# Optimization experiments

Hardware: AMD Instinct MI355X
Metric: run time of the kernel (lower is better)

Reference implementation:

```python
import jax, jax.numpy as jnp
import numpy as np

B = 8          # events per batch
NPB = 8192     # points per event (equal counts -> Nmax = NPB)
N = B * NPB
FEAT = 6
K = 128        # max_tokens
TOK = 768      # token_dim
KNN = 16       # k_neighbors
MLP_DIMS = [FEAT, 256, 512, 768, TOK]


def setup_inputs() -> dict:
    key = jax.random.key(0)
    ks = jax.random.split(key, 20)
    coords = jax.random.normal(ks[0], (N, 3), jnp.float32) * 5.0
    features = jax.random.normal(ks[1], (N, FEAT), jnp.float32)
    times = jax.random.uniform(ks[2], (N, 1), jnp.float32)
    # equal-sized, sorted batch ids (8192 points per event)
    batch_ids = jnp.repeat(jnp.arange(B, dtype=jnp.int32), NPB)
    inp = {"coords": coords, "features": features, "batch_ids": batch_ids, "times": times}
    # per-point MLP: 6 -> 256 -> 512 -> 768 -> 768 (last Linear has no ReLU)
    ki = 3
    for i in range(4):
        din, dout = MLP_DIMS[i], MLP_DIMS[i + 1]
        inp[f"W{i+1}"] = jax.random.normal(ks[ki], (din, dout), jnp.float32) / np.sqrt(din); ki += 1
        inp[f"b{i+1}"] = jnp.zeros((dout,), jnp.float32)
    # neighborhood MLP: 768 -> 768 -> 768
    inp["Wn1"] = jax.random.normal(ks[ki], (TOK, TOK), jnp.float32) / np.sqrt(TOK); ki += 1
    inp["bn1"] = jnp.zeros((TOK,), jnp.float32)
    inp["Wn2"] = jax.random.normal(ks[ki], (TOK, TOK), jnp.float32) / np.sqrt(TOK); ki += 1
    inp["bn2"] = jnp.zeros((TOK,), jnp.float32)
    return inp


def _forward(coords, features, batch_ids, times,
             W1, b1, W2, b2, W3, b3, W4, b4, Wn1, bn1, Wn2, bn2):
    INF = jnp.float32(jnp.inf)
    points4 = jnp.concatenate([coords[:, :3], times], axis=-1)  # [N,4] (x,y,z,t)
    # per-point MLP
    h = jax.nn.relu(features @ W1 + b1)
    h = jax.nn.relu(h @ W2 + b2)
    h = jax.nn.relu(h @ W3 + b3)
    feats = h @ W4 + b4                                          # [N,TOK]
    # ---- pack flat -> padded [B, NPB, *] ----
    counts = jnp.bincount(batch_ids, length=B)                   # [B]
    offsets = jnp.cumsum(counts) - counts
    pos = jnp.arange(N) - offsets[batch_ids]
    P = jnp.zeros((B, NPB, 4), points4.dtype).at[batch_ids, pos].set(points4)
    Fp = jnp.zeros((B, NPB, TOK), feats.dtype).at[batch_ids, pos].set(feats)
    valid = jnp.arange(NPB)[None, :] < counts[:, None]           # [B,NPB]
    # ---- small path: take first K points sorted by time ----
    tsort = jnp.where(valid, P[..., 3], INF)
    sorted_idx = jnp.argsort(tsort, axis=1)[:, :K]               # K <= NPB
    tokens_small = jnp.take_along_axis(Fp, sorted_idx[..., None], axis=1)
    cents_small = jnp.take_along_axis(P, sorted_idx[..., None], axis=1)
    masks_small = jnp.arange(K)[None, :] < jnp.minimum(counts, K)[:, None]
    tokens_small = tokens_small * masks_small[..., None]
    cents_small = cents_small * masks_small[..., None]
    # ---- batched FPS over 4D points ----
    min_d0 = jnp.where(valid, INF, 0.0)
    norms = jnp.where(valid, jnp.sum(P * P, axis=-1), -INF)
    first = jnp.argmax(norms, axis=1)                            # farthest-from-origin start
    barange = jnp.arange(B)
    def fps_step(carry, _):
        min_d, last = carry
        c = P[barange, last]                                     # [B,4]
        d = jnp.sum((P - c[:, None, :]) ** 2, axis=-1)
        d = jnp.where(valid, d, INF)
        min_d = jnp.minimum(min_d, d)
        return (min_d, jnp.argmax(min_d, axis=1)), last
    _, idx_seq = jax.lax.scan(fps_step, (min_d0, first), None, length=K)
    fps_idx = idx_seq.T                                          # [B,K]
    validK = jnp.arange(K)[None, :] < jnp.minimum(counts, K)[:, None]
    cents_large = jnp.take_along_axis(P, fps_idx[..., None], axis=1)  # [B,K,4]
    # ---- kNN pooling around centroids ----
    diff = cents_large[:, :, None, :] - P[:, None, :, :]         # [B,K,NPB,4]
    dists = jnp.sum(diff * diff, axis=-1)                        # [B,K,NPB]
    dists = jnp.where(valid[:, None, :], dists, INF)
    k_g = min(KNN, NPB)
    _, knn_idx = jax.lax.top_k(-dists, k_g)                      # smallest-k -> [B,K,k]
    knn_valid = jnp.take_along_axis(jnp.broadcast_to(valid[:, None, :], (B, K, NPB)), knn_idx, axis=2)
    neigh = jnp.take_along_axis(Fp[:, None, :, :], knn_idx[..., None], axis=2)  # [B,K,k,TOK]
    masked = jnp.where(knn_valid[..., None], neigh, -INF)
    pooled = jnp.max(masked, axis=2)
    pooled = jnp.where(jnp.isfinite(pooled), pooled, 0.0)
    tokens_large = jax.nn.relu(pooled @ Wn1 + bn1) @ Wn2 + bn2   # [B,K,TOK]
    # sort selected tokens by centroid time
    ctimes = jnp.where(validK, cents_large[..., 3], INF)
    order = jnp.argsort(ctimes, axis=1)
    tokens_large = jnp.take_along_axis(tokens_large, order[..., None], axis=1)
    cents_large = jnp.take_along_axis(cents_large, order[..., None], axis=1)
    masks_large = jnp.take_along_axis(validK, order, axis=1)
    tokens_large = tokens_large * masks_large[..., None]
    cents_large = cents_large * masks_large[..., None]
    # ---- select per-event path ----
    small = counts <= K
    tokens = jnp.where(small[:, None, None], tokens_small, tokens_large)
    cents = jnp.where(small[:, None, None], cents_small, cents_large)
    masks = jnp.where(small[:, None], masks_small, masks_large)
    return tokens, cents, masks


def reference(coords, features, batch_ids, times,
              W1, b1, W2, b2, W3, b3, W4, b4, Wn1, bn1, Wn2, bn2):
    return _forward(coords, features, batch_ids, times,
                    W1, b1, W2, b2, W3, b3, W4, b4, Wn1, bn1, Wn2, bn2)
```

## Files before the change

### kernel.cpp

```cpp
#include <hip/hip_runtime.h>
#include <hip/hip_bf16.h>


#define BEV 8
#define NPB 8192
#define FEAT 6
#define KTOK 128
#define TOK 768
#define KNN 16

typedef unsigned short ushort_t;
typedef unsigned long long u64;
typedef __bf16 bf16x8 __attribute__((ext_vector_type(8)));
typedef float f32x4 __attribute__((ext_vector_type(4)));
typedef float f32x2 __attribute__((ext_vector_type(2)));

__device__ __forceinline__ ushort_t f2b(float f) {
    union { float f; unsigned int i; } x; x.f = f;
    unsigned int i = x.i;
    unsigned int r = (i + 0x7FFFu + ((i >> 16) & 1u)) >> 16;
    return (ushort_t)r;
}

#define DPP_ROW_SHR1  0x111
#define DPP_ROW_SHR2  0x112
#define DPP_ROW_SHR4  0x114
#define DPP_ROW_SHR8  0x118
#define DPP_ROW_BC15  0x142
#define DPP_ROW_BC31  0x143

template <int CTRL>
__device__ __forceinline__ float dpp_fmax(float v) {
    int o = __builtin_amdgcn_update_dpp(__float_as_int(v), __float_as_int(v),
                                        CTRL, 0xf, 0xf, false);
    return fmaxf(v, __int_as_float(o));
}

template <int CTRL>
__device__ __forceinline__ u64 dpp_u64max(u64 k) {
    int lo = (int)(unsigned)(k & 0xFFFFFFFFu);
    int hi = (int)(unsigned)(k >> 32);
    unsigned olo = (unsigned)__builtin_amdgcn_update_dpp(lo, lo, CTRL, 0xf, 0xf, false);
    unsigned ohi = (unsigned)__builtin_amdgcn_update_dpp(hi, hi, CTRL, 0xf, 0xf, false);
    u64 o = ((u64)ohi << 32) | (u64)olo;
    return o > k ? o : k;
}

__global__ __launch_bounds__(256) void fill_kernel(float* __restrict__ out, int n) {
    int i = blockIdx.x * 256 + threadIdx.x;
    if (i < n) out[i] = 0.f;
}

__global__ __launch_bounds__(1024) void fps_kernel(
    const float* __restrict__ coords, const float* __restrict__ times,
    float* __restrict__ cents, int* __restrict__ pos,
    float* __restrict__ cents_out, float* __restrict__ masks_out)
{
#pragma clang fp contract(off)
    const int b = blockIdx.x;
    const int t = threadIdx.x;
    __shared__ u64   slotk[2][16];
    __shared__ __align__(16) float slotc[2][16][4];
    __shared__ float tarr[KTOK];
    __shared__ float carr[KTOK][4];
    f32x2 px[4], py[4], pz[4], pw[4], md[4];
    const long base = (long)b * NPB;
#pragma unroll
    for (int i = 0; i < 4; ++i) {
        long g = base + t * 8 + i * 2;
        px[i] = (f32x2){coords[g * 3 + 0], coords[(g + 1) * 3 + 0]};
        py[i] = (f32x2){coords[g * 3 + 1], coords[(g + 1) * 3 + 1]};
        pz[i] = (f32x2){coords[g * 3 + 2], coords[(g + 1) * 3 + 2]};
        pw[i] = (f32x2){times[g], times[g + 1]};
        md[i] = (f32x2){__builtin_inff(), __builtin_inff()};
    }
    const int wv = t >> 6, lane = t & 63;
    float cx = 0.f, cy = 0.f, cz = 0.f, cw = 0.f;
    for (int s = 0; s < KTOK; ++s) {
        float bv = -__builtin_inff(); int bi = t * 8;
        if (s == 0) {
#pragma unroll
            for (int i = 0; i < 4; ++i) {
                f32x2 n = ((px[i]*px[i] + py[i]*py[i]) + pz[i]*pz[i]) + pw[i]*pw[i];
                if (n[0] > bv) { bv = n[0]; bi = t * 8 + i * 2; }
                if (n[1] > bv) { bv = n[1]; bi = t * 8 + i * 2 + 1; }
            }
        } else {
            const f32x2 c2x = {cx, cx}, c2y = {cy, cy}, c2z = {cz, cz}, c2w = {cw, cw};
#pragma unroll
            for (int i = 0; i < 4; ++i) {
                f32x2 dx = px[i] - c2x, dy = py[i] - c2y;
                f32x2 dz = pz[i] - c2z, dw = pw[i] - c2w;
                f32x2 d = ((dx*dx + dy*dy) + dz*dz) + dw*dw;
                md[i] = __builtin_elementwise_min(md[i], d);
                if (md[i][0] > bv) { bv = md[i][0]; bi = t * 8 + i * 2; }
                if (md[i][1] > bv) { bv = md[i][1]; bi = t * 8 + i * 2 + 1; }
            }
        }
        float mvv = bv;
        mvv = dpp_fmax<DPP_ROW_SHR1>(mvv);
        mvv = dpp_fmax<DPP_ROW_SHR2>(mvv);
        mvv = dpp_fmax<DPP_ROW_SHR4>(mvv);
        mvv = dpp_fmax<DPP_ROW_SHR8>(mvv);
        mvv = dpp_fmax<DPP_ROW_BC15>(mvv);
        mvv = dpp_fmax<DPP_ROW_BC31>(mvv);
        const float mv = __int_as_float(__builtin_amdgcn_readlane(__float_as_int(mvv), 63));
        const u64 mask = __ballot(bv == mv);
        const int wl = __ffsll((long long)mask) - 1;
        const int p = s & 1;
        if (lane == wl) {
            slotk[p][wv] = ((u64)__float_as_uint(mv) << 32)
                         | (unsigned)(NPB - 1 - bi);
            const int ii = bi & 7;
            float sx = px[0][0], sy = py[0][0], sz = pz[0][0], sw = pw[0][0];
#pragma unroll
            for (int j = 1; j < 8; ++j)
                if (ii == j) { sx = px[j>>1][j&1]; sy = py[j>>1][j&1];
                               sz = pz[j>>1][j&1]; sw = pw[j>>1][j&1]; }
            slotc[p][wv][0] = sx; slotc[p][wv][1] = sy;
            slotc[p][wv][2] = sz; slotc[p][wv][3] = sw;
        }
        __syncthreads();
        u64 k1 = slotk[p][lane & 15];
        f32x4 c4 = *(const f32x4*)&slotc[p][lane & 15][0];
        k1 = dpp_u64max<DPP_ROW_SHR1>(k1);
        k1 = dpp_u64max<DPP_ROW_SHR2>(k1);
        k1 = dpp_u64max<DPP_ROW_SHR4>(k1);
        k1 = dpp_u64max<DPP_ROW_SHR8>(k1);
        const unsigned klo =
            (unsigned)__builtin_amdgcn_readlane((int)(unsigned)(k1 & 0xFFFFFFFFu), 15);
        const int widx = NPB - 1 - (int)klo;
        const int gw = widx >> 9;
        cx = __int_as_float(__builtin_amdgcn_readlane(__float_as_int(c4[0]), gw));
        cy = __int_as_float(__builtin_amdgcn_readlane(__float_as_int(c4[1]), gw));
        cz = __int_as_float(__builtin_amdgcn_readlane(__float_as_int(c4[2]), gw));
        cw = __int_as_float(__builtin_amdgcn_readlane(__float_as_int(c4[3]), gw));
        if (t == 0) {
            tarr[s] = cw;
            carr[s][0] = cx; carr[s][1] = cy; carr[s][2] = cz; carr[s][3] = cw;
        }
    }
    __syncthreads();
    if (t < KTOK) {
        const float ti = tarr[t];
        int rank = 0;
        for (int j = 0; j < KTOK; ++j) {
            float tj = tarr[j];
            if (tj < ti || (tj == ti && j < t)) ++rank;
        }
        rank &= (KTOK - 1);
        pos[b * KTOK + t] = rank;
        float* cc = &cents[(b * KTOK + t) * 4];
        cc[0] = carr[t][0]; cc[1] = carr[t][1];
        cc[2] = carr[t][2]; cc[3] = carr[t][3];
#pragma unroll
        for (int c = 0; c < 4; ++c)
            cents_out[(b * KTOK + rank) * 4 + c] = carr[t][c];
        masks_out[b * KTOK + t] = 1.0f;
    }
}

__global__ __launch_bounds__(256) void knn_kernel(
    const float* __restrict__ coords, const float* __restrict__ times,
    const float* __restrict__ cents, int* __restrict__ knn_idx)
{
#pragma clang fp contract(off)
    const int blk = blockIdx.x;
    const int b = blk >> 7;
    const int t = threadIdx.x;
    const float cx = cents[blk*4+0], cy = cents[blk*4+1];
    const float cz = cents[blk*4+2], cw = cents[blk*4+3];
    float d[32];
    const long base = (long)b * NPB;
#pragma unroll
    for (int i = 0; i < 32; ++i) {
        long g = base + t * 32 + i;
        float dx = coords[g*3+0] - cx;
        float dy = coords[g*3+1] - cy;
        float dz = coords[g*3+2] - cz;
        float dw = times[g] - cw;
        d[i] = ((dx*dx + dy*dy) + dz*dz) + dw*dw;
    }
    __shared__ float rv[4];
    __shared__ int   ri[4];
    const int wv = t >> 6, lane = t & 63;
    for (int pass = 0; pass < KNN; ++pass) {
        float bvv = __builtin_inff(); int bii = t * 32;
#pragma unroll
        for (int i = 0; i < 32; ++i)
            if (d[i] < bvv) { bvv = d[i]; bii = t * 32 + i; }
        for (int off = 1; off < 64; off <<= 1) {
            float ov = __shfl_xor(bvv, off);
            int   oi = __shfl_xor(bii, off);
            if (ov < bvv || (ov == bvv && oi < bii)) { bvv = ov; bii = oi; }
        }
        if (lane == 0) { rv[wv] = bvv; ri[wv] = bii; }
        __syncthreads();
        float gb = __builtin_inff(); int winner = 0;
        for (int wI = 0; wI < 4; ++wI) {
            float v = rv[wI]; int idx = ri[wI];
            if (v < gb || (v == gb && idx < winner)) { gb = v; winner = idx; }
        }
        winner &= (NPB - 1);
#pragma unroll
        for (int i = 0; i < 32; ++i)
            if (t * 32 + i == winner) d[i] = __builtin_inff();
        if (t == 0) knn_idx[blk * KNN + pass] = winner;
        __syncthreads();
    }
}

__global__ __launch_bounds__(256) void tc_all(
    const float* __restrict__ W2, ushort_t* __restrict__ Wt2,
    const float* __restrict__ W3, ushort_t* __restrict__ Wt3,
    const float* __restrict__ W4, ushort_t* __restrict__ Wt4)
{
    const float* in; ushort_t* out; int K, N;
    if (blockIdx.z == 0)      { in = W2; out = Wt2; K = 256; N = 512; }
    else if (blockIdx.z == 1) { in = W3; out = Wt3; K = 512; N = 768; }
    else                      { in = W4; out = Wt4; K = 768; N = 768; }
    if ((int)blockIdx.x * 32 >= N || (int)blockIdx.y * 32 >= K) return;
    __shared__ float tile[32][33];
    const int tx = threadIdx.x, ty = threadIdx.y;
#pragma unroll
    for (int r = 0; r < 4; ++r) {
        int y = blockIdx.y * 32 + ty + r * 8;
        tile[ty + r * 8][tx] = in[(long)y * N + blockIdx.x * 32 + tx];
    }
    __syncthreads();
    const int ko = blockIdx.y * 32 + tx;
#pragma unroll
    for (int r = 0; r < 4; ++r) {
        int no = blockIdx.x * 32 + ty + r * 8;
        out[(long)no * K + ko] = f2b(tile[tx][ty + r * 8]);
    }
}

#define PAD1 264
#define PAD2 520
#define PAD3 776
__global__ __launch_bounds__(256, 2) void mlp_fused(
    const float* __restrict__ features, const float* __restrict__ W1,
    const float* __restrict__ b1, const int* __restrict__ knn_idx,
    const ushort_t* __restrict__ Wt2, const float* __restrict__ b2,
    const ushort_t* __restrict__ Wt3, const float* __restrict__ b3,
    const ushort_t* __restrict__ Wt4, const float* __restrict__ b4,
    ushort_t* __restrict__ pooled)
{
    __shared__ __align__(16) ushort_t lds[35904];
    ushort_t* h1 = lds;
    ushort_t* h2 = lds + 8448;
    ushort_t* h3 = lds;
    ushort_t* Bs = lds + 25088;
    float*    feat = (float*)(lds + 35328);
    int*      pidx = (int*)(lds + 35840);

    const int bi = blockIdx.x;
    const int t = threadIdx.x;
    const int w = t >> 6, lane = t & 63;
    const int ln = lane & 15, q = lane >> 4;

    if (t < 32) {
        const int c = bi * 2 + (t >> 4);
        const int ev = c >> 7;
        pidx[t] = ev * NPB + (knn_idx[c * KNN + (t & 15)] & (NPB - 1));
    }
    __syncthreads();
    if (t < 192) {
        const int r = t / 6, f = t - r * 6;
        feat[r * 8 + f] = features[(long)pidx[r] * FEAT + f];
    }
    __syncthreads();
    {
        float wv[FEAT];
#pragma unroll
        for (int f = 0; f < FEAT; ++f) wv[f] = W1[f * 256 + t];
        const float bias = b1[t];
#pragma unroll
        for (int r = 0; r < 32; ++r) {
            float acc = 0.f;
#pragma unroll
            for (int f = 0; f < FEAT; ++f) acc += feat[r * 8 + f] * wv[f];
            h1[r * PAD1 + t] = f2b(fmaxf(acc + bias, 0.f));
        }
    }
    __syncthreads();

    {
        f32x4 acc[2][8];
#pragma unroll
        for (int m = 0; m < 2; ++m)
#pragma unroll
            for (int i = 0; i < 8; ++i) acc[m][i] = (f32x4){0,0,0,0};
        for (int k0 = 0; k0 < 256; k0 += 32) {
            bf16x8 af[2];
#pragma unroll
            for (int m = 0; m < 2; ++m)
                af[m] = *(const bf16x8*)(&h1[(m * 16 + ln) * PAD1 + k0 + q * 8]);
#pragma unroll
            for (int np = 0; np < 2; ++np) {
                __syncthreads();
#pragma unroll
                for (int i = 0; i < 4; ++i) {
                    int e = t + i * 256, n = e >> 2, sk = e & 3;
                    *(uint4*)(&Bs[n * 40 + sk * 8]) =
                        *(const uint4*)(Wt2 + (long)(np * 256 + n) * 256 + k0 + sk * 8);
                }
                __syncthreads();
#pragma unroll
                for (int j = 0; j < 4; ++j) {
                    bf16x8 bf = *(const bf16x8*)(&Bs[((w * 4 + j) * 16 + ln) * 40 + q * 8]);
#pragma unroll
                    for (int m = 0; m < 2; ++m)
                        acc[m][np * 4 + j] = __builtin_amdgcn_mfma_f32_16x16x32_bf16(af[m], bf, acc[m][np * 4 + j], 0, 0, 0);
                }
            }
        }
        __syncthreads();
#pragma unroll
        for (int np = 0; np < 2; ++np)
#pragma unroll
            for (int j = 0; j < 4; ++j) {
                const int col = np * 256 + (w * 4 + j) * 16 + ln;
                const float bias = b2[col];
#pragma unroll
                for (int m = 0; m < 2; ++m)
#pragma unroll
                    for (int r = 0; r < 4; ++r)
                        h2[(m * 16 + q * 4 + r) * PAD2 + col] = f2b(fmaxf(acc[m][np * 4 + j][r] + bias, 0.f));
            }
    }
    __syncthreads();

    {
        f32x4 acc[2][12];
#pragma unroll
        for (int m = 0; m < 2; ++m)
#pragma unroll
            for (int i = 0; i < 12; ++i) acc[m][i] = (f32x4){0,0,0,0};
        for (int k0 = 0; k0 < 512; k0 += 32) {
            bf16x8 af[2];
#pragma unroll
            for (int m = 0; m < 2; ++m)
                af[m] = *(const bf16x8*)(&h2[(m * 16 + ln) * PAD2 + k0 + q * 8]);
#pragma unroll
            for (int np = 0; np < 3; ++np) {
                __syncthreads();
#pragma unroll
                for (int i = 0; i < 4; ++i) {
                    int e = t + i * 256, n = e >> 2, sk = e & 3;
                    *(uint4*)(&Bs[n * 40 + sk * 8]) =
                        *(const uint4*)(Wt3 + (long)(np * 256 + n) * 512 + k0 + sk * 8);
                }
                __syncthreads();
#pragma unroll
                for (int j = 0; j < 4; ++j) {
                    bf16x8 bf = *(const bf16x8*)(&Bs[((w * 4 + j) * 16 + ln) * 40 + q * 8]);
#pragma unroll
                    for (int m = 0; m < 2; ++m)
                        acc[m][np * 4 + j] = __builtin_amdgcn_mfma_f32_16x16x32_bf16(af[m], bf, acc[m][np * 4 + j], 0, 0, 0);
                }
            }
        }
        __syncthreads();
#pragma unroll
        for (int np = 0; np < 3; ++np)
#pragma unroll
            for (int j = 0; j < 4; ++j) {
                const int col = np * 256 + (w * 4 + j) * 16 + ln;
                const float bias = b3[col];
#pragma unroll
                for (int m = 0; m < 2; ++m)
#pragma unroll
                    for (int r = 0; r < 4; ++r)
                        h3[(m * 16 + q * 4 + r) * PAD3 + col] = f2b(fmaxf(acc[m][np * 4 + j][r] + bias, 0.f));
            }
    }
    __syncthreads();

    {
        f32x4 acc[2][12];
#pragma unroll
        for (int m = 0; m < 2; ++m)
#pragma unroll
            for (int i = 0; i < 12; ++i) acc[m][i] = (f32x4){0,0,0,0};
        for (int k0 = 0; k0 < 768; k0 += 32) {
            bf16x8 af[2];
#pragma unroll
            for (int m = 0; m < 2; ++m)
                af[m] = *(const bf16x8*)(&h3[(m * 16 + ln) * PAD3 + k0 + q * 8]);
#pragma unroll
            for (int np = 0; np < 3; ++np) {
                __syncthreads();
#pragma unroll
                for (int i = 0; i < 4; ++i) {
                    int e = t + i * 256, n = e >> 2, sk = e & 3;
                    *(uint4*)(&Bs[n * 40 + sk * 8]) =
                        *(const uint4*)(Wt4 + (long)(np * 256 + n) * 768 + k0 + sk * 8);
                }
                __syncthreads();
#pragma unroll
                for (int j = 0; j < 4; ++j) {
                    bf16x8 bf = *(const bf16x8*)(&Bs[((w * 4 + j) * 16 + ln) * 40 + q * 8]);
#pragma unroll
                    for (int m = 0; m < 2; ++m)
                        acc[m][np * 4 + j] = __builtin_amdgcn_mfma_f32_16x16x32_bf16(af[m], bf, acc[m][np * 4 + j], 0, 0, 0);
                }
            }
        }
#pragma unroll
        for (int np = 0; np < 3; ++np)
#pragma unroll
            for (int j = 0; j < 4; ++j) {
                const int col = np * 256 + (w * 4 + j) * 16 + ln;
#pragma unroll
                for (int m = 0; m < 2; ++m) {
                    float v = fmaxf(fmaxf(acc[m][np * 4 + j][0], acc[m][np * 4 + j][1]),
                                    fmaxf(acc[m][np * 4 + j][2], acc[m][np * 4 + j][3]));
                    v = fmaxf(v, __shfl_xor(v, 16));
                    v = fmaxf(v, __shfl_xor(v, 32));
                    if (q == 0)
                        pooled[(long)(bi * 2 + m) * TOK + col] = f2b(v + b4[col]);
                }
            }
    }
}

template<int EPI, int RELU, int F32OUT>
__global__ __launch_bounds__(256) void gemm64_kn(
    const ushort_t* __restrict__ A, const float* __restrict__ B,
    const float* __restrict__ bias, void* __restrict__ Cv,
    int M, int N, int Kd, const int* __restrict__ pos)
{
    __shared__ __align__(16) ushort_t As[64 * 40];
    __shared__ __align__(16) ushort_t Bsh[64 * 40];
    ushort_t* Cb = (ushort_t*)Cv;
    float*    Cf = (float*)Cv;
    const int tid = threadIdx.x;
    const int m0 = blockIdx.x * 64;
    const int n0 = blockIdx.y * 64;
    const int w = tid >> 6, lane = tid & 63;
    const int ln = lane & 15, q = lane >> 4;
    f32x4 acc[4];
#pragma unroll
    for (int ni = 0; ni < 4; ++ni) acc[ni] = (f32x4){0.f, 0.f, 0.f, 0.f};

    const int ar = tid >> 2, as0 = (tid & 3) * 8;
    const int kk = tid >> 4, nn = (tid & 15) * 4;

    for (int k0 = 0; k0 < Kd; k0 += 32) {
        __syncthreads();
        uint4 a0 = *(const uint4*)(A + (long)(m0 + ar) * Kd + k0 + as0);
        float4 f0 = *(const float4*)(B + (long)(k0 + kk)      * N + n0 + nn);
        float4 f1 = *(const float4*)(B + (long)(k0 + kk + 16) * N + n0 + nn);
        *(uint4*)(&As[ar * 40 + as0]) = a0;
        float e0[4] = {f0.x, f0.y, f0.z, f0.w};
        float e1[4] = {f1.x, f1.y, f1.z, f1.w};
#pragma unroll
        for (int j = 0; j < 4; ++j) Bsh[(nn + j) * 40 + kk]      = f2b(e0[j]);
#pragma unroll
        for (int j = 0; j < 4; ++j) Bsh[(nn + j) * 40 + kk + 16] = f2b(e1[j]);
        __syncthreads();
        bf16x8 af = *(const bf16x8*)(&As[(w * 16 + ln) * 40 + q * 8]);
#pragma unroll
        for (int ni = 0; ni < 4; ++ni) {
            bf16x8 bf = *(const bf16x8*)(&Bsh[(ni * 16 + ln) * 40 + q * 8]);
            acc[ni] = __builtin_amdgcn_mfma_f32_16x16x32_bf16(af, bf, acc[ni], 0, 0, 0);
        }
    }

#pragma unroll
    for (int ni = 0; ni < 4; ++ni) {
        const int col = n0 + ni * 16 + ln;
        const float bv = bias[col];
#pragma unroll
        for (int r = 0; r < 4; ++r) {
            const int row = m0 + w * 16 + q * 4 + r;
            float v = acc[ni][r] + bv;
            if (EPI == 0) {
                if (RELU) v = fmaxf(v, 0.f);
                if (F32OUT) Cf[(long)row * N + col] = v;
                else        Cb[(long)row * N + col] = f2b(v);
            } else {
                const int orow = (row & ~(KTOK - 1)) + (pos[row] & (KTOK - 1));
                if (F32OUT) Cf[(long)orow * N + col] = v;
                else        Cb[(long)orow * N + col] = f2b(v);
            }
        }
    }
}

extern "C" void kernel_launch(void* const* d_in, const int* in_sizes, int n_in,
                              void* d_out, int out_size, void* d_ws, size_t ws_size,
                              hipStream_t stream)
{
    const float* coords   = (const float*)d_in[0];
    const float* features = (const float*)d_in[1];
    const float* times    = (const float*)d_in[3];
    const float* W1  = (const float*)d_in[4];
    const float* b1  = (const float*)d_in[5];
    const float* W2  = (const float*)d_in[6];
    const float* b2  = (const float*)d_in[7];
    const float* W3  = (const float*)d_in[8];
    const float* b3  = (const float*)d_in[9];
    const float* W4  = (const float*)d_in[10];
    const float* b4  = (const float*)d_in[11];
    const float* Wn1 = (const float*)d_in[12];
    const float* bn1 = (const float*)d_in[13];
    const float* Wn2 = (const float*)d_in[14];
    const float* bn2 = (const float*)d_in[15];

    char* ws = (char*)d_ws;
    float*    cents   = (float*)(ws + 0);
    int*      pos     = (int*)(ws + 16384);
    int*      knn_idx = (int*)(ws + 20480);
    ushort_t* t1      = (ushort_t*)(ws + 86016);
    ushort_t* pooled  = (ushort_t*)(ws + 1658880);
    ushort_t* Wt2b    = (ushort_t*)(ws + 3231744);
    ushort_t* Wt3b    = (ushort_t*)(ws + 3493888);
    ushort_t* Wt4b    = (ushort_t*)(ws + 4280320);
    const long WS_NEED = 5459968;

    float* tokens_out = (float*)d_out;
    float* cents_out  = tokens_out + 786432;
    float* masks_out  = tokens_out + 790528;

    if ((long)ws_size < WS_NEED) {
        fill_kernel<<<(791552 + 255) / 256, 256, 0, stream>>>(tokens_out, 791552);
        return;
    }

    tc_all<<<dim3(24, 24, 3), dim3(32, 8), 0, stream>>>(W2, Wt2b, W3, Wt3b, W4, Wt4b);

    fps_kernel<<<BEV, 1024, 0, stream>>>(coords, times, cents, pos, cents_out, masks_out);
    knn_kernel<<<BEV * KTOK, 256, 0, stream>>>(coords, times, cents, knn_idx);

    mlp_fused<<<512, 256, 0, stream>>>(features, W1, b1, knn_idx,
                                       Wt2b, b2, Wt3b, b3, Wt4b, b4, pooled);

    gemm64_kn<0,1,0><<<dim3(16, 12), 256, 0, stream>>>(pooled, Wn1, bn1, t1, 1024, 768, 768, nullptr);
    gemm64_kn<2,0,1><<<dim3(16, 12), 256, 0, stream>>>(t1, Wn2, bn2, tokens_out, 1024, 768, 768, pos);
}
```

Baseline: 478.3 us.

## Split FPS across four blocks per event with global atomic key exchange

```diff
diff --git a/kernel.cpp b/kernel.cpp
--- a/kernel.cpp
+++ b/kernel.cpp
@@ -8,6 +8,8 @@
 #define KTOK 128
 #define TOK 768
 #define KNN 16
+#define FPS_S 4
+#define FPS_KSTRIDE 16
 
 typedef unsigned short ushort_t;
 typedef unsigned long long u64;
@@ -53,49 +55,43 @@
 
 __global__ __launch_bounds__(1024) void fps_kernel(
     const float* __restrict__ coords, const float* __restrict__ times,
-    float* __restrict__ cents, int* __restrict__ pos,
+    float* __restrict__ cents, int* __restrict__ pos, u64* __restrict__ keys,
     float* __restrict__ cents_out, float* __restrict__ masks_out)
 {
 #pragma clang fp contract(off)
-    const int b = blockIdx.x;
+    const int blk = blockIdx.x;
+    const int b = blk >> 2, bl = blk & (FPS_S - 1);
     const int t = threadIdx.x;
     __shared__ u64   slotk[2][16];
-    __shared__ __align__(16) float slotc[2][16][4];
     __shared__ float tarr[KTOK];
     __shared__ float carr[KTOK][4];
-    f32x2 px[4], py[4], pz[4], pw[4], md[4];
     const long base = (long)b * NPB;
-#pragma unroll
-    for (int i = 0; i < 4; ++i) {
-        long g = base + t * 8 + i * 2;
-        px[i] = (f32x2){coords[g * 3 + 0], coords[(g + 1) * 3 + 0]};
-        py[i] = (f32x2){coords[g * 3 + 1], coords[(g + 1) * 3 + 1]};
-        pz[i] = (f32x2){coords[g * 3 + 2], coords[(g + 1) * 3 + 2]};
-        pw[i] = (f32x2){times[g], times[g + 1]};
-        md[i] = (f32x2){__builtin_inff(), __builtin_inff()};
-    }
+    const int g0 = bl * (NPB / FPS_S) + t * 2;
+    f32x2 px, py, pz, pw, md;
+    {
+        long g = base + g0;
+        px = (f32x2){coords[g * 3 + 0], coords[(g + 1) * 3 + 0]};
+        py = (f32x2){coords[g * 3 + 1], coords[(g + 1) * 3 + 1]};
+        pz = (f32x2){coords[g * 3 + 2], coords[(g + 1) * 3 + 2]};
+        pw = (f32x2){times[g], times[g + 1]};
+    }
+    md = (f32x2){__builtin_inff(), __builtin_inff()};
     const int wv = t >> 6, lane = t & 63;
     float cx = 0.f, cy = 0.f, cz = 0.f, cw = 0.f;
     for (int s = 0; s < KTOK; ++s) {
-        float bv = -__builtin_inff(); int bi = t * 8;
+        float bv; int bi = g0;
         if (s == 0) {
-#pragma unroll
-            for (int i = 0; i < 4; ++i) {
-                f32x2 n = ((px[i]*px[i] + py[i]*py[i]) + pz[i]*pz[i]) + pw[i]*pw[i];
-                if (n[0] > bv) { bv = n[0]; bi = t * 8 + i * 2; }
-                if (n[1] > bv) { bv = n[1]; bi = t * 8 + i * 2 + 1; }
-            }
+            f32x2 n = ((px*px + py*py) + pz*pz) + pw*pw;
+            bv = n[0];
+            if (n[1] > bv) { bv = n[1]; bi = g0 + 1; }
         } else {
             const f32x2 c2x = {cx, cx}, c2y = {cy, cy}, c2z = {cz, cz}, c2w = {cw, cw};
-#pragma unroll
-            for (int i = 0; i < 4; ++i) {
-                f32x2 dx = px[i] - c2x, dy = py[i] - c2y;
-                f32x2 dz = pz[i] - c2z, dw = pw[i] - c2w;
-                f32x2 d = ((dx*dx + dy*dy) + dz*dz) + dw*dw;
-                md[i] = __builtin_elementwise_min(md[i], d);
-                if (md[i][0] > bv) { bv = md[i][0]; bi = t * 8 + i * 2; }
-                if (md[i][1] > bv) { bv = md[i][1]; bi = t * 8 + i * 2 + 1; }
-            }
+            f32x2 dx = px - c2x, dy = py - c2y;
+            f32x2 dz = pz - c2z, dw = pw - c2w;
+            f32x2 d = ((dx*dx + dy*dy) + dz*dz) + dw*dw;
+            md = __builtin_elementwise_min(md, d);
+            bv = md[0];
+            if (md[1] > bv) { bv = md[1]; bi = g0 + 1; }
         }
         float mvv = bv;
         mvv = dpp_fmax<DPP_ROW_SHR1>(mvv);
@@ -108,40 +104,45 @@
         const u64 mask = __ballot(bv == mv);
         const int wl = __ffsll((long long)mask) - 1;
         const int p = s & 1;
-        if (lane == wl) {
-            slotk[p][wv] = ((u64)__float_as_uint(mv) << 32)
+        if (lane == wl)
+            slotk[p][wv] = ((u64)(__float_as_uint(mv) + 1u) << 32)
                          | (unsigned)(NPB - 1 - bi);
-            const int ii = bi & 7;
-            float sx = px[0][0], sy = py[0][0], sz = pz[0][0], sw = pw[0][0];
-#pragma unroll
-            for (int j = 1; j < 8; ++j)
-                if (ii == j) { sx = px[j>>1][j&1]; sy = py[j>>1][j&1];
-                               sz = pz[j>>1][j&1]; sw = pw[j>>1][j&1]; }
-            slotc[p][wv][0] = sx; slotc[p][wv][1] = sy;
-            slotc[p][wv][2] = sz; slotc[p][wv][3] = sw;
-        }
         __syncthreads();
         u64 k1 = slotk[p][lane & 15];
-        f32x4 c4 = *(const f32x4*)&slotc[p][lane & 15][0];
         k1 = dpp_u64max<DPP_ROW_SHR1>(k1);
         k1 = dpp_u64max<DPP_ROW_SHR2>(k1);
         k1 = dpp_u64max<DPP_ROW_SHR4>(k1);
         k1 = dpp_u64max<DPP_ROW_SHR8>(k1);
         const unsigned klo =
             (unsigned)__builtin_amdgcn_readlane((int)(unsigned)(k1 & 0xFFFFFFFFu), 15);
-        const int widx = NPB - 1 - (int)klo;
-        const int gw = widx >> 9;
-        cx = __int_as_float(__builtin_amdgcn_readlane(__float_as_int(c4[0]), gw));
-        cy = __int_as_float(__builtin_amdgcn_readlane(__float_as_int(c4[1]), gw));
-        cz = __int_as_float(__builtin_amdgcn_readlane(__float_as_int(c4[2]), gw));
-        cw = __int_as_float(__builtin_amdgcn_readlane(__float_as_int(c4[3]), gw));
+        const unsigned khi =
+            (unsigned)__builtin_amdgcn_readlane((int)(unsigned)(k1 >> 32), 15);
+        u64* kq = keys + (long)(s * BEV + b) * FPS_KSTRIDE;
+        if (t == 0)
+            __hip_atomic_store(&kq[bl], ((u64)khi << 32) | (u64)klo,
+                               __ATOMIC_RELAXED, __HIP_MEMORY_SCOPE_AGENT);
+        u64 q0, q1, q2, q3;
+        for (;;) {
+            q0 = __hip_atomic_load(&kq[0], __ATOMIC_RELAXED, __HIP_MEMORY_SCOPE_AGENT);
+            q1 = __hip_atomic_load(&kq[1], __ATOMIC_RELAXED, __HIP_MEMORY_SCOPE_AGENT);
+            q2 = __hip_atomic_load(&kq[2], __ATOMIC_RELAXED, __HIP_MEMORY_SCOPE_AGENT);
+            q3 = __hip_atomic_load(&kq[3], __ATOMIC_RELAXED, __HIP_MEMORY_SCOPE_AGENT);
+            if (q0 && q1 && q2 && q3) break;
+        }
+        u64 ka = q0 > q1 ? q0 : q1;
+        u64 kb2 = q2 > q3 ? q2 : q3;
+        u64 kg = ka > kb2 ? ka : kb2;
+        const int widx = NPB - 1 - (int)(unsigned)(kg & 0xFFFFFFFFu);
+        const long gc = base + widx;
+        cx = coords[gc * 3 + 0]; cy = coords[gc * 3 + 1];
+        cz = coords[gc * 3 + 2]; cw = times[gc];
         if (t == 0) {
             tarr[s] = cw;
             carr[s][0] = cx; carr[s][1] = cy; carr[s][2] = cz; carr[s][3] = cw;
         }
     }
     __syncthreads();
-    if (t < KTOK) {
+    if (bl == 0 && t < KTOK) {
         const float ti = tarr[t];
         int rank = 0;
         for (int j = 0; j < KTOK; ++j) {
@@ -213,8 +214,15 @@
 __global__ __launch_bounds__(256) void tc_all(
     const float* __restrict__ W2, ushort_t* __restrict__ Wt2,
     const float* __restrict__ W3, ushort_t* __restrict__ Wt3,
-    const float* __restrict__ W4, ushort_t* __restrict__ Wt4)
+    const float* __restrict__ W4, ushort_t* __restrict__ Wt4,
+    u64* __restrict__ keys)
 {
+    if (blockIdx.z == 3) {
+        int id = ((int)blockIdx.y * 24 + (int)blockIdx.x) * 256
+               + (int)threadIdx.y * 32 + (int)threadIdx.x;
+        if (id < KTOK * BEV * FPS_KSTRIDE) keys[id] = 0ull;
+        return;
+    }
     const float* in; ushort_t* out; int K, N;
     if (blockIdx.z == 0)      { in = W2; out = Wt2; K = 256; N = 512; }
     else if (blockIdx.z == 1) { in = W3; out = Wt3; K = 512; N = 768; }
@@ -519,7 +527,8 @@
     ushort_t* Wt2b    = (ushort_t*)(ws + 3231744);
     ushort_t* Wt3b    = (ushort_t*)(ws + 3493888);
     ushort_t* Wt4b    = (ushort_t*)(ws + 4280320);
-    const long WS_NEED = 5459968;
+    u64*      fpskeys = (u64*)(ws + 5459968);
+    const long WS_NEED = 5459968 + 131072;
 
     float* tokens_out = (float*)d_out;
     float* cents_out  = tokens_out + 786432;
@@ -530,9 +539,10 @@
         return;
     }
 
-    tc_all<<<dim3(24, 24, 3), dim3(32, 8), 0, stream>>>(W2, Wt2b, W3, Wt3b, W4, Wt4b);
-
-    fps_kernel<<<BEV, 1024, 0, stream>>>(coords, times, cents, pos, cents_out, masks_out);
+    tc_all<<<dim3(24, 24, 4), dim3(32, 8), 0, stream>>>(W2, Wt2b, W3, Wt3b, W4, Wt4b, fpskeys);
+
+    fps_kernel<<<BEV * FPS_S, 1024, 0, stream>>>(coords, times, cents, pos, fpskeys,
+                                                 cents_out, masks_out);
     knn_kernel<<<BEV * KTOK, 256, 0, stream>>>(coords, times, cents, knn_idx);
 
     mlp_fused<<<512, 256, 0, stream>>>(features, W1, b1, knn_idx,
```

New measurement: 506.8 us. +6.0%, slower.

## Simplify FPS argmax and fold weight transpose into KNN launch

Applied to the files above, without the earlier changes.

```diff
diff --git a/kernel.cpp b/kernel.cpp
--- a/kernel.cpp
+++ b/kernel.cpp
@@ -60,7 +60,6 @@
     const int b = blockIdx.x;
     const int t = threadIdx.x;
     __shared__ u64   slotk[2][16];
-    __shared__ __align__(16) float slotc[2][16][4];
     __shared__ float tarr[KTOK];
     __shared__ float carr[KTOK][4];
     f32x2 px[4], py[4], pz[4], pw[4], md[4];
@@ -77,14 +76,11 @@
     const int wv = t >> 6, lane = t & 63;
     float cx = 0.f, cy = 0.f, cz = 0.f, cw = 0.f;
     for (int s = 0; s < KTOK; ++s) {
-        float bv = -__builtin_inff(); int bi = t * 8;
+        f32x2 v[4];
         if (s == 0) {
 #pragma unroll
-            for (int i = 0; i < 4; ++i) {
-                f32x2 n = ((px[i]*px[i] + py[i]*py[i]) + pz[i]*pz[i]) + pw[i]*pw[i];
-                if (n[0] > bv) { bv = n[0]; bi = t * 8 + i * 2; }
-                if (n[1] > bv) { bv = n[1]; bi = t * 8 + i * 2 + 1; }
-            }
+            for (int i = 0; i < 4; ++i)
+                v[i] = ((px[i]*px[i] + py[i]*py[i]) + pz[i]*pz[i]) + pw[i]*pw[i];
         } else {
             const f32x2 c2x = {cx, cx}, c2y = {cy, cy}, c2z = {cz, cz}, c2w = {cw, cw};
 #pragma unroll
@@ -93,10 +89,13 @@
                 f32x2 dz = pz[i] - c2z, dw = pw[i] - c2w;
                 f32x2 d = ((dx*dx + dy*dy) + dz*dz) + dw*dw;
                 md[i] = __builtin_elementwise_min(md[i], d);
-                if (md[i][0] > bv) { bv = md[i][0]; bi = t * 8 + i * 2; }
-                if (md[i][1] > bv) { bv = md[i][1]; bi = t * 8 + i * 2 + 1; }
-            }
-        }
+                v[i] = md[i];
+            }
+        }
+        f32x2 m01 = __builtin_elementwise_max(v[0], v[1]);
+        f32x2 m23 = __builtin_elementwise_max(v[2], v[3]);
+        f32x2 mm  = __builtin_elementwise_max(m01, m23);
+        const float bv = fmaxf(mm[0], mm[1]);
         float mvv = bv;
         mvv = dpp_fmax<DPP_ROW_SHR1>(mvv);
         mvv = dpp_fmax<DPP_ROW_SHR2>(mvv);
@@ -109,20 +108,15 @@
         const int wl = __ffsll((long long)mask) - 1;
         const int p = s & 1;
         if (lane == wl) {
+            int bi = t * 8;
+#pragma unroll
+            for (int j = 7; j >= 0; --j)
+                if (v[j >> 1][j & 1] == mv) bi = t * 8 + j;
             slotk[p][wv] = ((u64)__float_as_uint(mv) << 32)
                          | (unsigned)(NPB - 1 - bi);
-            const int ii = bi & 7;
-            float sx = px[0][0], sy = py[0][0], sz = pz[0][0], sw = pw[0][0];
-#pragma unroll
-            for (int j = 1; j < 8; ++j)
-                if (ii == j) { sx = px[j>>1][j&1]; sy = py[j>>1][j&1];
-                               sz = pz[j>>1][j&1]; sw = pw[j>>1][j&1]; }
-            slotc[p][wv][0] = sx; slotc[p][wv][1] = sy;
-            slotc[p][wv][2] = sz; slotc[p][wv][3] = sw;
         }
         __syncthreads();
         u64 k1 = slotk[p][lane & 15];
-        f32x4 c4 = *(const f32x4*)&slotc[p][lane & 15][0];
         k1 = dpp_u64max<DPP_ROW_SHR1>(k1);
         k1 = dpp_u64max<DPP_ROW_SHR2>(k1);
         k1 = dpp_u64max<DPP_ROW_SHR4>(k1);
@@ -130,11 +124,9 @@
         const unsigned klo =
             (unsigned)__builtin_amdgcn_readlane((int)(unsigned)(k1 & 0xFFFFFFFFu), 15);
         const int widx = NPB - 1 - (int)klo;
-        const int gw = widx >> 9;
-        cx = __int_as_float(__builtin_amdgcn_readlane(__float_as_int(c4[0]), gw));
-        cy = __int_as_float(__builtin_amdgcn_readlane(__float_as_int(c4[1]), gw));
-        cz = __int_as_float(__builtin_amdgcn_readlane(__float_as_int(c4[2]), gw));
-        cw = __int_as_float(__builtin_amdgcn_readlane(__float_as_int(c4[3]), gw));
+        const long gc = base + widx;
+        cx = coords[gc * 3 + 0]; cy = coords[gc * 3 + 1];
+        cz = coords[gc * 3 + 2]; cw = times[gc];
         if (t == 0) {
             tarr[s] = cw;
             carr[s][0] = cx; carr[s][1] = cy; carr[s][2] = cz; carr[s][3] = cw;
@@ -160,12 +152,42 @@
     }
 }
 
-__global__ __launch_bounds__(256) void knn_kernel(
+__global__ __launch_bounds__(256) void knn_tc(
     const float* __restrict__ coords, const float* __restrict__ times,
-    const float* __restrict__ cents, int* __restrict__ knn_idx)
+    const float* __restrict__ cents, int* __restrict__ knn_idx,
+    const float* __restrict__ W2, ushort_t* __restrict__ Wt2,
+    const float* __restrict__ W3, ushort_t* __restrict__ Wt3,
+    const float* __restrict__ W4, ushort_t* __restrict__ Wt4)
 {
 #pragma clang fp contract(off)
+    __shared__ float tile[32][33];
+    __shared__ float rv[4];
+    __shared__ int   ri[4];
     const int blk = blockIdx.x;
+    if (blk >= BEV * KTOK) {
+        const int id = blk - BEV * KTOK;
+        const float* in; ushort_t* out; int K, N, bx, by;
+        if (id < 128)      { in = W2; out = Wt2; K = 256; N = 512;
+                             bx = id & 15; by = id >> 4; }
+        else if (id < 512) { in = W3; out = Wt3; K = 512; N = 768;
+                             int r = id - 128; bx = r % 24; by = r / 24; }
+        else               { in = W4; out = Wt4; K = 768; N = 768;
+                             int r = id - 512; bx = r % 24; by = r / 24; }
+        const int tt = threadIdx.x, tx = tt & 31, ty = tt >> 5;
+#pragma unroll
+        for (int r = 0; r < 4; ++r) {
+            int y = by * 32 + ty + r * 8;
+            tile[ty + r * 8][tx] = in[(long)y * N + bx * 32 + tx];
+        }
+        __syncthreads();
+        const int ko = by * 32 + tx;
+#pragma unroll
+        for (int r = 0; r < 4; ++r) {
+            int no = bx * 32 + ty + r * 8;
+            out[(long)no * K + ko] = f2b(tile[tx][ty + r * 8]);
+        }
+        return;
+    }
     const int b = blk >> 7;
     const int t = threadIdx.x;
     const float cx = cents[blk*4+0], cy = cents[blk*4+1];
@@ -181,8 +203,6 @@
         float dw = times[g] - cw;
         d[i] = ((dx*dx + dy*dy) + dz*dz) + dw*dw;
     }
-    __shared__ float rv[4];
-    __shared__ int   ri[4];
     const int wv = t >> 6, lane = t & 63;
     for (int pass = 0; pass < KNN; ++pass) {
         float bvv = __builtin_inff(); int bii = t * 32;
@@ -207,32 +227,6 @@
             if (t * 32 + i == winner) d[i] = __builtin_inff();
         if (t == 0) knn_idx[blk * KNN + pass] = winner;
         __syncthreads();
-    }
-}
-
-__global__ __launch_bounds__(256) void tc_all(
-    const float* __restrict__ W2, ushort_t* __restrict__ Wt2,
-    const float* __restrict__ W3, ushort_t* __restrict__ Wt3,
-    const float* __restrict__ W4, ushort_t* __restrict__ Wt4)
-{
-    const float* in; ushort_t* out; int K, N;
-    if (blockIdx.z == 0)      { in = W2; out = Wt2; K = 256; N = 512; }
-    else if (blockIdx.z == 1) { in = W3; out = Wt3; K = 512; N = 768; }
-    else                      { in = W4; out = Wt4; K = 768; N = 768; }
-    if ((int)blockIdx.x * 32 >= N || (int)blockIdx.y * 32 >= K) return;
-    __shared__ float tile[32][33];
-    const int tx = threadIdx.x, ty = threadIdx.y;
-#pragma unroll
-    for (int r = 0; r < 4; ++r) {
-        int y = blockIdx.y * 32 + ty + r * 8;
-        tile[ty + r * 8][tx] = in[(long)y * N + blockIdx.x * 32 + tx];
-    }
-    __syncthreads();
-    const int ko = blockIdx.y * 32 + tx;
-#pragma unroll
-    for (int r = 0; r < 4; ++r) {
-        int no = blockIdx.x * 32 + ty + r * 8;
-        out[(long)no * K + ko] = f2b(tile[tx][ty + r * 8]);
     }
 }
 
@@ -530,10 +524,11 @@
         return;
     }
 
-    tc_all<<<dim3(24, 24, 3), dim3(32, 8), 0, stream>>>(W2, Wt2b, W3, Wt3b, W4, Wt4b);
-
-    fps_kernel<<<BEV, 1024, 0, stream>>>(coords, times, cents, pos, cents_out, masks_out);
-    knn_kernel<<<BEV * KTOK, 256, 0, stream>>>(coords, times, cents, knn_idx);
+    fps_kernel<<<BEV, 1024, 0, stream>>>(coords, times, cents, pos,
+                                         cents_out, masks_out);
+
+    knn_tc<<<BEV * KTOK + 1088, 256, 0, stream>>>(coords, times, cents, knn_idx,
+                                                  W2, Wt2b, W3, Wt3b, W4, Wt4b);
 
     mlp_fused<<<512, 256, 0, stream>>>(features, W1, b1, knn_idx,
                                        Wt2b, b2, Wt3b, b3, Wt4b, b4, pooled);
```

Result: faster. 432.7 us (-9.5%).
